# Performance work log

Hardware: AMD Instinct MI355X
Metric: run time of the kernel (lower is better)

## Reference

```python
import jax, jax.numpy as jnp
import numpy as np

K = 5
TAU = 2.0
EPS = 1e-8
SLOPE = 0.2  # LeakyReLU negative slope
BASE = jnp.array([-2.0, -1.0, 0.0, 1.0, 2.0], dtype=jnp.float32)


def _leaky(x):
    return jnp.where(x >= 0, x, SLOPE * x)


def _bilinear1d(feat, x):
    """1D bilinear sample, equivalent to F.grid_sample on an [B,C,1,L] image
    with grid_y=0, padding_mode='border', align_corners=True.
    feat: [B,C,L], x: [B,M] normalized coords in [-1,1]. Returns [B,C,M]."""
    L = feat.shape[-1]
    ix = jnp.clip((x + 1.0) * 0.5 * (L - 1), 0.0, float(L - 1))  # border clamp
    x0 = jnp.floor(ix)
    w = (ix - x0)[:, None, :]  # [B,1,M]
    i0 = jnp.clip(x0.astype(jnp.int32), 0, L - 1)
    i1 = jnp.clip(i0 + 1, 0, L - 1)
    f0 = jnp.take_along_axis(feat, i0[:, None, :], axis=2)
    f1 = jnp.take_along_axis(feat, i1[:, None, :], axis=2)
    return f0 * (1.0 - w) + f1 * w


def setup_inputs() -> dict:
    key = jax.random.key(0)
    ks = jax.random.split(key, 10)
    B, C, Lin, N, H = 4, 256, 4096, 8192, 64
    out_dim = 1 + 1 + K + K  # 12
    feat_1d = jax.random.normal(ks[0], (B, C, Lin), dtype=jnp.float32)
    coords_1d = jax.random.uniform(ks[1], (B, N, 1), minval=-1.0, maxval=1.0, dtype=jnp.float32)
    cell_1d = jnp.full((B, N, 1), 2.0 / Lin, dtype=jnp.float32) * (1.0 + 0.1 * jax.random.uniform(ks[2], (B, N, 1)))
    in_dim = C + 2
    # NOTE: original zero-inits the last linear; we use small random weights to
    # exercise the full computation (non-degenerate offsets/gates).
    W1 = jax.random.normal(ks[3], (in_dim, H), dtype=jnp.float32) * (1.0 / np.sqrt(in_dim))
    b1 = jax.random.normal(ks[4], (H,), dtype=jnp.float32) * 0.01
    Wr = jax.random.normal(ks[5], (H, H), dtype=jnp.float32) * (1.0 / np.sqrt(H))
    br = jax.random.normal(ks[6], (H,), dtype=jnp.float32) * 0.01
    W3 = jax.random.normal(ks[7], (H, out_dim), dtype=jnp.float32) * 0.1
    b3 = jax.random.normal(ks[8], (out_dim,), dtype=jnp.float32) * 0.01
    return {"feat_1d": feat_1d, "coords_1d": coords_1d, "cell_1d": cell_1d,
            "W1": W1, "b1": b1, "Wr": Wr, "br": br, "W3": W3, "b3": b3}


def reference(feat_1d, coords_1d, cell_1d, W1, b1, Wr, br, W3, b3):
    B, C, Lin = feat_1d.shape
    N = coords_1d.shape[1]
    x = coords_1d[..., 0]  # [B,N]
    # anchor features at query coords
    f_anchor = _bilinear1d(feat_1d, x).transpose(0, 2, 1)  # [B,N,C]
    rin = jnp.concatenate([f_anchor, coords_1d, cell_1d], axis=-1)  # [B,N,C+2]
    # router MLP: Linear -> LeakyReLU -> ResidualBlock -> Linear
    h = _leaky(rin @ W1 + b1)
    h = _leaky(h + (h @ Wr + br))
    out = h @ W3 + b3  # [B,N,12]
    r_raw = out[..., 0:1]
    sigma_raw = out[..., 1:2]
    res_raw = out[..., 2:2 + K]
    gate_raw = out[..., 2 + K:2 + 2 * K]
    r = jnp.clip(jax.nn.softplus(r_raw) + 0.3, 0.3, 2.0)          # [B,N,1]
    sigma = jnp.clip(jax.nn.softplus(sigma_raw) + 0.5, 0.5, 3.0)  # [B,N,1]
    res = jnp.tanh(res_raw) * 0.5                                  # [B,N,K]
    off = r * BASE + res                                           # [B,N,K] pixel-unit offsets
    scale_x = 2.0 / max(Lin - 1, 1)
    deform_x = x[:, :, None] + off * scale_x                       # [B,N,K] normalized
    f = _bilinear1d(feat_1d, deform_x.reshape(B, N * K))           # [B,C,N*K]
    f = f.reshape(B, C, N, K).transpose(0, 2, 3, 1)                # [B,N,K,C]
    w_geo = jnp.exp(-0.5 * off ** 2 / ((sigma * TAU) ** 2 + EPS))  # [B,N,K]
    w = w_geo * jax.nn.sigmoid(gate_raw)
    w = w / (w.sum(axis=-1, keepdims=True) + EPS)
    out_feat = jnp.einsum('bnkc,bnk->bnc', f, w)                   # [B,N,C]
    return out_feat
```

## Files before the change

### kernel.cpp

```cpp
#include <hip/hip_runtime.h>
#include <math.h>

#define KK 5
#define C_DIM 256
#define LIN 4096
#define B_DIM 4
#define N_PTS 8192
#define PTS 32
#define NBUCK (B_DIM * LIN)

typedef short short8 __attribute__((ext_vector_type(8)));
typedef float f32x4  __attribute__((ext_vector_type(4)));

__device__ __forceinline__ float leaky(float v) { return v >= 0.0f ? v : 0.2f * v; }
__device__ __forceinline__ float softplus_f(float v) { return v > 20.0f ? v : log1pf(expf(v)); }
__device__ __forceinline__ float bflo(unsigned u) { return __uint_as_float(u << 16); }
__device__ __forceinline__ float bfhi(unsigned u) { return __uint_as_float(u & 0xFFFF0000u); }
__device__ __forceinline__ ushort f2bf(float f) {
    unsigned u = __float_as_uint(f);
    u += 0x7FFFu + ((u >> 16) & 1u);
    return (ushort)(u >> 16);
}
__device__ __forceinline__ float bf2f(ushort h) { return __uint_as_float((unsigned)h << 16); }
__device__ __forceinline__ int anchor_key(const float* coords, int pt) {
    float x = coords[pt];
    float ix = fminf(fmaxf((x + 1.0f) * 0.5f * (float)(LIN - 1), 0.0f), (float)(LIN - 1));
    return (pt >> 13) * LIN + (int)ix;
}

__global__ __launch_bounds__(256) void prep_weights(
    const float* __restrict__ W1, const float* __restrict__ Wr,
    ushort* __restrict__ W1t_hi, ushort* __restrict__ W1t_lo,
    ushort* __restrict__ Wrt_hi, ushort* __restrict__ Wrt_lo)
{
    int i = blockIdx.x * 256 + threadIdx.x;
    if (i < 64 * 264) {
        int j = i / 264, k = i % 264;
        float v = (k < 256) ? W1[(size_t)k * 64 + j] : 0.0f;
        ushort hi = f2bf(v);
        W1t_hi[i] = hi;
        W1t_lo[i] = f2bf(v - bf2f(hi));
    } else {
        int i2 = i - 64 * 264;
        if (i2 < 64 * 72) {
            int j = i2 / 72, k = i2 % 72;
            float v = (k < 64) ? Wr[(size_t)k * 64 + j] : 0.0f;
            ushort hi = f2bf(v);
            Wrt_hi[i2] = hi;
            Wrt_lo[i2] = f2bf(v - bf2f(hi));
        }
    }
}

__global__ __launch_bounds__(256) void sort_count(
    const float* __restrict__ coords, unsigned* __restrict__ hist)
{
    int pt = blockIdx.x * 256 + threadIdx.x;
    atomicAdd(&hist[anchor_key(coords, pt)], 1u);
}

__global__ __launch_bounds__(256) void sort_scan(
    const unsigned* __restrict__ hist, unsigned* __restrict__ offs)
{
    __shared__ unsigned base[256];
    int t = threadIdx.x;
    unsigned s = 0;
    for (int i = 0; i < NBUCK / 256; i++) s += hist[t * (NBUCK / 256) + i];
    base[t] = s;
    __syncthreads();
    if (t == 0) {
        unsigned run = 0;
        for (int i = 0; i < 256; i++) { unsigned v = base[i]; base[i] = run; run += v; }
    }
    __syncthreads();
    unsigned run = base[t];
    for (int i = 0; i < NBUCK / 256; i++) {
        int idx = t * (NBUCK / 256) + i;
        offs[idx] = run;
        run += hist[idx];
    }
}

__global__ __launch_bounds__(256) void sort_scatter(
    const float* __restrict__ coords, unsigned* __restrict__ offs,
    int* __restrict__ perm)
{
    int pt = blockIdx.x * 256 + threadIdx.x;
    unsigned pos = atomicAdd(&offs[anchor_key(coords, pt)], 1u);
    perm[pos] = pt;
}

__global__ __launch_bounds__(256) void transpose_kernel(
    const float* __restrict__ feat, ushort* __restrict__ feat_t)
{
    __shared__ float tile[32][33];
    int b  = blockIdx.z;
    int l0 = blockIdx.x * 32;
    int c0 = blockIdx.y * 32;
    const float* src = feat + (size_t)b * C_DIM * LIN;
    ushort* dst = feat_t + (size_t)b * LIN * C_DIM;
    int tx = threadIdx.x, ty = threadIdx.y;
#pragma unroll
    for (int i = 0; i < 4; i++)
        tile[ty + i * 8][tx] = src[(size_t)(c0 + ty + i * 8) * LIN + (l0 + tx)];
    __syncthreads();
#pragma unroll
    for (int i = 0; i < 4; i++)
        dst[(size_t)(l0 + ty + i * 8) * C_DIM + (c0 + tx)] = f2bf(tile[tx][ty + i * 8]);
}

__global__ __launch_bounds__(256) void mlp_kernel(
    const ushort* __restrict__ feat_t,
    const float* __restrict__ coords,
    const float* __restrict__ cell,
    const float* __restrict__ W1, const float* __restrict__ b1,
    const float* __restrict__ br,
    const float* __restrict__ W3, const float* __restrict__ b3,
    const ushort* __restrict__ W1t_hi, const ushort* __restrict__ W1t_lo,
    const ushort* __restrict__ Wrt_hi, const ushort* __restrict__ Wrt_lo,
    float* __restrict__ params)
{
    __shared__ ushort Ah[PTS][264], Al[PTS][264];
    __shared__ ushort H1h[PTS][72], H1l[PTS][72];
    __shared__ float  H2[PTS][68];
    __shared__ float  outs[PTS][12];
    __shared__ float  xs[PTS], cls[PTS];

    const int t = threadIdx.x;
    const int base = blockIdx.x * PTS;
    const int bb = base >> 13;
    const ushort* fb = feat_t + (size_t)bb * LIN * C_DIM;

    {
        int p = t >> 3, l8 = t & 7;
        int pt = base + p;
        float x = coords[pt];
        float ix = fminf(fmaxf((x + 1.0f) * 0.5f * (float)(LIN - 1), 0.0f), (float)(LIN - 1));
        float x0 = floorf(ix);
        int i0 = min((int)x0, LIN - 1);
        int i1 = min(i0 + 1, LIN - 1);
        float fr = ix - x0, om = 1.0f - fr;
        if (l8 == 0) { xs[p] = x; cls[p] = cell[pt]; }
        const ushort* r0 = fb + (size_t)i0 * C_DIM;
        const ushort* r1 = fb + (size_t)i1 * C_DIM;
#pragma unroll
        for (int q = 0; q < 4; q++) {
            int c = l8 * 8 + q * 64;
            uint4 u0 = *(const uint4*)(r0 + c);
            uint4 u1 = *(const uint4*)(r1 + c);
            float v[8];
            v[0] = bflo(u0.x) * om + bflo(u1.x) * fr;
            v[1] = bfhi(u0.x) * om + bfhi(u1.x) * fr;
            v[2] = bflo(u0.y) * om + bflo(u1.y) * fr;
            v[3] = bfhi(u0.y) * om + bfhi(u1.y) * fr;
            v[4] = bflo(u0.z) * om + bflo(u1.z) * fr;
            v[5] = bfhi(u0.z) * om + bfhi(u1.z) * fr;
            v[6] = bflo(u0.w) * om + bflo(u1.w) * fr;
            v[7] = bfhi(u0.w) * om + bfhi(u1.w) * fr;
            ushort hv[8], lv[8];
#pragma unroll
            for (int e = 0; e < 8; e++) {
                hv[e] = f2bf(v[e]);
                lv[e] = f2bf(v[e] - bf2f(hv[e]));
            }
            *(uint4*)&Ah[p][c] = *(uint4*)hv;
            *(uint4*)&Al[p][c] = *(uint4*)lv;
        }
    }
    __syncthreads();

    const int wave = t >> 6, lane = t & 63;
    const int cr = lane & 15;
    const int kb = lane >> 4;
    const int jcol = wave * 16 + cr;

    f32x4 acc0 = {0.f, 0.f, 0.f, 0.f}, acc1 = acc0;
    {
        const ushort* B1h = W1t_hi + (size_t)jcol * 264;
        const ushort* B1l = W1t_lo + (size_t)jcol * 264;
#pragma unroll
        for (int k0 = 0; k0 < 256; k0 += 32) {
            int ko = k0 + kb * 8;
            short8 a0h = *(const short8*)&Ah[cr][ko];
            short8 a0l = *(const short8*)&Al[cr][ko];
            short8 a1h = *(const short8*)&Ah[16 + cr][ko];
            short8 a1l = *(const short8*)&Al[16 + cr][ko];
            short8 bh = *(const short8*)(B1h + ko);
            short8 bl = *(const short8*)(B1l + ko);
            acc0 = __builtin_amdgcn_mfma_f32_16x16x32_bf16(a0h, bh, acc0, 0, 0, 0);
            acc0 = __builtin_amdgcn_mfma_f32_16x16x32_bf16(a0h, bl, acc0, 0, 0, 0);
            acc0 = __builtin_amdgcn_mfma_f32_16x16x32_bf16(a0l, bh, acc0, 0, 0, 0);
            acc1 = __builtin_amdgcn_mfma_f32_16x16x32_bf16(a1h, bh, acc1, 0, 0, 0);
            acc1 = __builtin_amdgcn_mfma_f32_16x16x32_bf16(a1h, bl, acc1, 0, 0, 0);
            acc1 = __builtin_amdgcn_mfma_f32_16x16x32_bf16(a1l, bh, acc1, 0, 0, 0);
        }
    }
    float h1a[4], h1b[4];
    {
        float wx = W1[(size_t)256 * 64 + jcol];
        float wc = W1[(size_t)257 * 64 + jcol];
        float bb1 = b1[jcol];
#pragma unroll
        for (int r = 0; r < 4; r++) {
            int p0 = kb * 4 + r;
            float v0 = leaky(acc0[r] + xs[p0] * wx + cls[p0] * wc + bb1);
            h1a[r] = v0;
            ushort hi0 = f2bf(v0);
            H1h[p0][jcol] = hi0;
            H1l[p0][jcol] = f2bf(v0 - bf2f(hi0));
            int p1 = 16 + p0;
            float v1 = leaky(acc1[r] + xs[p1] * wx + cls[p1] * wc + bb1);
            h1b[r] = v1;
            ushort hi1 = f2bf(v1);
            H1h[p1][jcol] = hi1;
            H1l[p1][jcol] = f2bf(v1 - bf2f(hi1));
        }
    }
    __syncthreads();

    f32x4 r0 = {0.f, 0.f, 0.f, 0.f}, r1 = r0;
    {
        const ushort* B2h = Wrt_hi + (size_t)jcol * 72;
        const ushort* B2l = Wrt_lo + (size_t)jcol * 72;
#pragma unroll
        for (int k0 = 0; k0 < 64; k0 += 32) {
            int ko = k0 + kb * 8;
            short8 a0h = *(const short8*)&H1h[cr][ko];
            short8 a0l = *(const short8*)&H1l[cr][ko];
            short8 a1h = *(const short8*)&H1h[16 + cr][ko];
            short8 a1l = *(const short8*)&H1l[16 + cr][ko];
            short8 bh = *(const short8*)(B2h + ko);
            short8 bl = *(const short8*)(B2l + ko);
            r0 = __builtin_amdgcn_mfma_f32_16x16x32_bf16(a0h, bh, r0, 0, 0, 0);
            r0 = __builtin_amdgcn_mfma_f32_16x16x32_bf16(a0h, bl, r0, 0, 0, 0);
            r0 = __builtin_amdgcn_mfma_f32_16x16x32_bf16(a0l, bh, r0, 0, 0, 0);
            r1 = __builtin_amdgcn_mfma_f32_16x16x32_bf16(a1h, bh, r1, 0, 0, 0);
            r1 = __builtin_amdgcn_mfma_f32_16x16x32_bf16(a1h, bl, r1, 0, 0, 0);
            r1 = __builtin_amdgcn_mfma_f32_16x16x32_bf16(a1l, bh, r1, 0, 0, 0);
        }
        float brv = br[jcol];
#pragma unroll
        for (int r = 0; r < 4; r++) {
            int p0 = kb * 4 + r;
            H2[p0][jcol]      = leaky(h1a[r] + r0[r] + brv);
            H2[16 + p0][jcol] = leaky(h1b[r] + r1[r] + brv);
        }
    }
    __syncthreads();

    {
        int p = t & 31;
        int o = t >> 5;
        for (int oo = o; oo < 12; oo += 8) {
            float acc = b3[oo];
#pragma unroll 4
            for (int l = 0; l < 64; l++)
                acc = fmaf(H2[p][l], W3[(size_t)l * 12 + oo], acc);
            outs[p][oo] = acc;
        }
    }
    __syncthreads();

    if (t < PTS) {
        int pt = base + t;
        float x = xs[t];
        float r = softplus_f(outs[t][0]) + 0.3f;
        r = fminf(fmaxf(r, 0.3f), 2.0f);
        float sg = softplus_f(outs[t][1]) + 0.5f;
        sg = fminf(fmaxf(sg, 0.5f), 3.0f);
        float denom = (sg * 2.0f) * (sg * 2.0f) + 1e-8f;
        const float BASEv[KK] = {-2.0f, -1.0f, 0.0f, 1.0f, 2.0f};
        float ixk[KK], wk[KK];
        float wsum = 0.0f;
#pragma unroll
        for (int k = 0; k < KK; k++) {
            float res = tanhf(outs[t][2 + k]) * 0.5f;
            float off = r * BASEv[k] + res;
            float dx = x + off * (2.0f / (float)(LIN - 1));
            float ix = (dx + 1.0f) * 0.5f * (float)(LIN - 1);
            ix = fminf(fmaxf(ix, 0.0f), (float)(LIN - 1));
            float gate = outs[t][2 + KK + k];
            float wgeo = expf(-0.5f * off * off / denom);
            float sig = 1.0f / (1.0f + expf(-gate));
            float w = wgeo * sig;
            ixk[k] = ix; wk[k] = w; wsum += w;
        }
        float inv = 1.0f / (wsum + 1e-8f);
        float* pp = params + (size_t)pt * 10;
#pragma unroll
        for (int k = 0; k < KK; k++) {
            pp[k]     = ixk[k];
            pp[5 + k] = wk[k] * inv;
        }
    }
}

__global__ __launch_bounds__(256) void gather_kernel(
    const ushort* __restrict__ feat_t, const float* __restrict__ params,
    const int* __restrict__ perm, float* __restrict__ out)
{
    int t = threadIdx.x;
    int p = t >> 5;
    int lane = t & 31;
    int pt = perm[blockIdx.x * 8 + p];
    int b = pt >> 13;
    const float* pp = params + (size_t)pt * 10;
    const ushort* fb = feat_t + (size_t)b * LIN * C_DIM;
    int c = lane * 8;
    float a0 = 0, a1 = 0, a2 = 0, a3 = 0, a4 = 0, a5 = 0, a6 = 0, a7 = 0;
#pragma unroll
    for (int k = 0; k < KK; k++) {
        float ix = pp[k];
        float w  = pp[5 + k];
        float x0 = floorf(ix);
        int i0 = (int)x0;
        int i1 = min(i0 + 1, LIN - 1);
        float fr = ix - x0;
        uint4 u0 = *(const uint4*)(fb + (size_t)i0 * C_DIM + c);
        uint4 u1 = *(const uint4*)(fb + (size_t)i1 * C_DIM + c);
        float w0 = w * (1.0f - fr), w1 = w * fr;
        a0 = fmaf(w0, bflo(u0.x), fmaf(w1, bflo(u1.x), a0));
        a1 = fmaf(w0, bfhi(u0.x), fmaf(w1, bfhi(u1.x), a1));
        a2 = fmaf(w0, bflo(u0.y), fmaf(w1, bflo(u1.y), a2));
        a3 = fmaf(w0, bfhi(u0.y), fmaf(w1, bfhi(u1.y), a3));
        a4 = fmaf(w0, bflo(u0.z), fmaf(w1, bflo(u1.z), a4));
        a5 = fmaf(w0, bfhi(u0.z), fmaf(w1, bfhi(u1.z), a5));
        a6 = fmaf(w0, bflo(u0.w), fmaf(w1, bflo(u1.w), a6));
        a7 = fmaf(w0, bfhi(u0.w), fmaf(w1, bfhi(u1.w), a7));
    }
    float* op = out + (size_t)pt * C_DIM + c;
    *(float4*)op       = make_float4(a0, a1, a2, a3);
    *(float4*)(op + 4) = make_float4(a4, a5, a6, a7);
}

extern "C" void kernel_launch(void* const* d_in, const int* in_sizes, int n_in,
                              void* d_out, int out_size, void* d_ws, size_t ws_size,
                              hipStream_t stream) {
    const float* feat   = (const float*)d_in[0];
    const float* coords = (const float*)d_in[1];
    const float* cell   = (const float*)d_in[2];
    const float* W1 = (const float*)d_in[3];
    const float* b1 = (const float*)d_in[4];
    const float* Wr = (const float*)d_in[5];
    const float* br = (const float*)d_in[6];
    const float* W3 = (const float*)d_in[7];
    const float* b3 = (const float*)d_in[8];
    float* out = (float*)d_out;

    char* ws = (char*)d_ws;
    ushort* feat_t = (ushort*)ws;
    ws += (size_t)B_DIM * LIN * C_DIM * 2;
    float* params = (float*)ws;
    ws += (size_t)B_DIM * N_PTS * 10 * 4;
    ushort* W1t_hi = (ushort*)ws; ws += 64 * 264 * 2;
    ushort* W1t_lo = (ushort*)ws; ws += 64 * 264 * 2;
    ushort* Wrt_hi = (ushort*)ws; ws += 64 * 72 * 2;
    ushort* Wrt_lo = (ushort*)ws; ws += 64 * 72 * 2;
    ws = (char*)(((uintptr_t)ws + 255) & ~(uintptr_t)255);
    unsigned* hist = (unsigned*)ws; ws += NBUCK * 4;
    unsigned* offs = (unsigned*)ws; ws += NBUCK * 4;
    int* perm      = (int*)ws;      ws += (size_t)B_DIM * N_PTS * 4;

    int nPts = B_DIM * N_PTS;

    hipMemsetAsync(hist, 0, NBUCK * 4, stream);
    sort_count<<<nPts / 256, 256, 0, stream>>>(coords, hist);
    sort_scan<<<1, 256, 0, stream>>>(hist, offs);
    sort_scatter<<<nPts / 256, 256, 0, stream>>>(coords, offs, perm);

    prep_weights<<<(64 * 264 + 64 * 72 + 255) / 256, 256, 0, stream>>>(
        W1, Wr, W1t_hi, W1t_lo, Wrt_hi, Wrt_lo);

    dim3 tb(32, 8);
    dim3 tg(LIN / 32, C_DIM / 32, B_DIM);
    transpose_kernel<<<tg, tb, 0, stream>>>(feat, feat_t);

    mlp_kernel<<<nPts / PTS, 256, 0, stream>>>(feat_t, coords, cell,
                                               W1, b1, br, W3, b3,
                                               W1t_hi, W1t_lo, Wrt_hi, Wrt_lo,
                                               params);

    gather_kernel<<<nPts / 8, 256, 0, stream>>>(feat_t, params, perm, out);
}
```

Measured before the change: 144.1 us.

## Stage feature windows in LDS for gather and process MLP in sorted order

The gather kernel now gives each block a 32-row window of the transposed feature map, plus a 5-row halo, and stages it in shared memory. Each block then processes the sorted points whose anchor falls in that window, using a new prefix array written by the scan kernel. This aims to replace scattered global/L2 row fetches with LDS reads. The MLP kernel also reads points through the sort permutation for better anchor-row locality, and the transpose now writes packed bf16 pairs over a wider channel tile. Risks are load imbalance across windows with uneven point density, and the halo assumption that offsets stay within about 5 pixels.

```diff
diff --git a/kernel.cpp b/kernel.cpp
--- a/kernel.cpp
+++ b/kernel.cpp
@@ -8,6 +8,8 @@
 #define N_PTS 8192
 #define PTS 32
 #define NBUCK (B_DIM * LIN)
+#define WROWS 32
+#define SROWS 44
 
 typedef short short8 __attribute__((ext_vector_type(8)));
 typedef float f32x4  __attribute__((ext_vector_type(4)));
@@ -60,7 +62,8 @@
 }
 
 __global__ __launch_bounds__(256) void sort_scan(
-    const unsigned* __restrict__ hist, unsigned* __restrict__ offs)
+    const unsigned* __restrict__ hist, unsigned* __restrict__ offs,
+    unsigned* __restrict__ pfx)
 {
     __shared__ unsigned base[256];
     int t = threadIdx.x;
@@ -77,8 +80,10 @@
     for (int i = 0; i < NBUCK / 256; i++) {
         int idx = t * (NBUCK / 256) + i;
         offs[idx] = run;
+        pfx[idx] = run;
         run += hist[idx];
     }
+    if (t == 255) pfx[NBUCK] = run;
 }
 
 __global__ __launch_bounds__(256) void sort_scatter(
@@ -93,20 +98,24 @@
 __global__ __launch_bounds__(256) void transpose_kernel(
     const float* __restrict__ feat, ushort* __restrict__ feat_t)
 {
-    __shared__ float tile[32][33];
+    __shared__ float tile[64][33];
     int b  = blockIdx.z;
     int l0 = blockIdx.x * 32;
-    int c0 = blockIdx.y * 32;
+    int c0 = blockIdx.y * 64;
     const float* src = feat + (size_t)b * C_DIM * LIN;
-    ushort* dst = feat_t + (size_t)b * LIN * C_DIM;
+    unsigned* dst = (unsigned*)(feat_t + (size_t)b * LIN * C_DIM);
     int tx = threadIdx.x, ty = threadIdx.y;
 #pragma unroll
-    for (int i = 0; i < 4; i++)
+    for (int i = 0; i < 8; i++)
         tile[ty + i * 8][tx] = src[(size_t)(c0 + ty + i * 8) * LIN + (l0 + tx)];
     __syncthreads();
 #pragma unroll
-    for (int i = 0; i < 4; i++)
-        dst[(size_t)(l0 + ty + i * 8) * C_DIM + (c0 + tx)] = f2bf(tile[tx][ty + i * 8]);
+    for (int i = 0; i < 4; i++) {
+        int l = ty + i * 8;
+        unsigned lo = f2bf(tile[2 * tx][l]);
+        unsigned hi = f2bf(tile[2 * tx + 1][l]);
+        dst[((size_t)(l0 + l) * C_DIM + c0) / 2 + tx] = lo | (hi << 16);
+    }
 }
 
 __global__ __launch_bounds__(256) void mlp_kernel(
@@ -118,6 +127,7 @@
     const float* __restrict__ W3, const float* __restrict__ b3,
     const ushort* __restrict__ W1t_hi, const ushort* __restrict__ W1t_lo,
     const ushort* __restrict__ Wrt_hi, const ushort* __restrict__ Wrt_lo,
+    const int* __restrict__ perm,
     float* __restrict__ params)
 {
     __shared__ ushort Ah[PTS][264], Al[PTS][264];
@@ -133,7 +143,7 @@
 
     {
         int p = t >> 3, l8 = t & 7;
-        int pt = base + p;
+        int pt = perm[base + p];
         float x = coords[pt];
         float ix = fminf(fmaxf((x + 1.0f) * 0.5f * (float)(LIN - 1), 0.0f), (float)(LIN - 1));
         float x0 = floorf(ix);
@@ -262,7 +272,7 @@
     __syncthreads();
 
     if (t < PTS) {
-        int pt = base + t;
+        int pt = perm[base + t];
         float x = xs[t];
         float r = softplus_f(outs[t][0]) + 0.3f;
         r = fminf(fmaxf(r, 0.3f), 2.0f);
@@ -297,40 +307,54 @@
 
 __global__ __launch_bounds__(256) void gather_kernel(
     const ushort* __restrict__ feat_t, const float* __restrict__ params,
-    const int* __restrict__ perm, float* __restrict__ out)
-{
-    int t = threadIdx.x;
-    int p = t >> 5;
-    int lane = t & 31;
-    int pt = perm[blockIdx.x * 8 + p];
-    int b = pt >> 13;
-    const float* pp = params + (size_t)pt * 10;
-    const ushort* fb = feat_t + (size_t)b * LIN * C_DIM;
-    int c = lane * 8;
-    float a0 = 0, a1 = 0, a2 = 0, a3 = 0, a4 = 0, a5 = 0, a6 = 0, a7 = 0;
-#pragma unroll
-    for (int k = 0; k < KK; k++) {
-        float ix = pp[k];
-        float w  = pp[5 + k];
-        float x0 = floorf(ix);
-        int i0 = (int)x0;
-        int i1 = min(i0 + 1, LIN - 1);
-        float fr = ix - x0;
-        uint4 u0 = *(const uint4*)(fb + (size_t)i0 * C_DIM + c);
-        uint4 u1 = *(const uint4*)(fb + (size_t)i1 * C_DIM + c);
-        float w0 = w * (1.0f - fr), w1 = w * fr;
-        a0 = fmaf(w0, bflo(u0.x), fmaf(w1, bflo(u1.x), a0));
-        a1 = fmaf(w0, bfhi(u0.x), fmaf(w1, bfhi(u1.x), a1));
-        a2 = fmaf(w0, bflo(u0.y), fmaf(w1, bflo(u1.y), a2));
-        a3 = fmaf(w0, bfhi(u0.y), fmaf(w1, bfhi(u1.y), a3));
-        a4 = fmaf(w0, bflo(u0.z), fmaf(w1, bflo(u1.z), a4));
-        a5 = fmaf(w0, bfhi(u0.z), fmaf(w1, bfhi(u1.z), a5));
-        a6 = fmaf(w0, bflo(u0.w), fmaf(w1, bflo(u1.w), a6));
-        a7 = fmaf(w0, bfhi(u0.w), fmaf(w1, bfhi(u1.w), a7));
-    }
-    float* op = out + (size_t)pt * C_DIM + c;
-    *(float4*)op       = make_float4(a0, a1, a2, a3);
-    *(float4*)(op + 4) = make_float4(a4, a5, a6, a7);
+    const int* __restrict__ perm, const unsigned* __restrict__ pfx,
+    float* __restrict__ out)
+{
+    __shared__ uint4 sm[SROWS * 32];
+    const int t = threadIdx.x;
+    const int wpb = LIN / WROWS;
+    const int b  = blockIdx.x / wpb;
+    const int w0 = (blockIdx.x % wpb) * WROWS;
+    const int rowLo = max(0, w0 - 5);
+    const int rowHi = min(LIN, w0 + WROWS + 6);
+    const int nrows = rowHi - rowLo;
+
+    const uint4* src = (const uint4*)(feat_t + ((size_t)b * LIN + rowLo) * C_DIM);
+    for (int i = t; i < nrows * 32; i += 256) sm[i] = src[i];
+    __syncthreads();
+
+    const unsigned ptStart = pfx[b * LIN + w0];
+    const unsigned ptEnd   = pfx[b * LIN + w0 + WROWS];
+    const int lane = t & 31;
+
+    for (unsigned ip = ptStart + (t >> 5); ip < ptEnd; ip += 8) {
+        int pt = perm[ip];
+        const float* pp = params + (size_t)pt * 10;
+        float a0 = 0, a1 = 0, a2 = 0, a3 = 0, a4 = 0, a5 = 0, a6 = 0, a7 = 0;
+#pragma unroll
+        for (int k = 0; k < KK; k++) {
+            float ix = pp[k];
+            float w  = pp[5 + k];
+            float x0 = floorf(ix);
+            int i0 = (int)x0;
+            int i1 = min(i0 + 1, LIN - 1);
+            float fr = ix - x0;
+            uint4 u0 = sm[(i0 - rowLo) * 32 + lane];
+            uint4 u1 = sm[(i1 - rowLo) * 32 + lane];
+            float w0f = w * (1.0f - fr), w1f = w * fr;
+            a0 = fmaf(w0f, bflo(u0.x), fmaf(w1f, bflo(u1.x), a0));
+            a1 = fmaf(w0f, bfhi(u0.x), fmaf(w1f, bfhi(u1.x), a1));
+            a2 = fmaf(w0f, bflo(u0.y), fmaf(w1f, bflo(u1.y), a2));
+            a3 = fmaf(w0f, bfhi(u0.y), fmaf(w1f, bfhi(u1.y), a3));
+            a4 = fmaf(w0f, bflo(u0.z), fmaf(w1f, bflo(u1.z), a4));
+            a5 = fmaf(w0f, bfhi(u0.z), fmaf(w1f, bfhi(u1.z), a5));
+            a6 = fmaf(w0f, bflo(u0.w), fmaf(w1f, bflo(u1.w), a6));
+            a7 = fmaf(w0f, bfhi(u0.w), fmaf(w1f, bfhi(u1.w), a7));
+        }
+        float* op = out + (size_t)pt * C_DIM + lane * 8;
+        *(float4*)op       = make_float4(a0, a1, a2, a3);
+        *(float4*)(op + 4) = make_float4(a4, a5, a6, a7);
+    }
 }
 
 extern "C" void kernel_launch(void* const* d_in, const int* in_sizes, int n_in,
@@ -359,26 +383,29 @@
     ws = (char*)(((uintptr_t)ws + 255) & ~(uintptr_t)255);
     unsigned* hist = (unsigned*)ws; ws += NBUCK * 4;
     unsigned* offs = (unsigned*)ws; ws += NBUCK * 4;
+    unsigned* pfx  = (unsigned*)ws; ws += (NBUCK + 1) * 4;
+    ws = (char*)(((uintptr_t)ws + 255) & ~(uintptr_t)255);
     int* perm      = (int*)ws;      ws += (size_t)B_DIM * N_PTS * 4;
 
     int nPts = B_DIM * N_PTS;
 
     hipMemsetAsync(hist, 0, NBUCK * 4, stream);
     sort_count<<<nPts / 256, 256, 0, stream>>>(coords, hist);
-    sort_scan<<<1, 256, 0, stream>>>(hist, offs);
+    sort_scan<<<1, 256, 0, stream>>>(hist, offs, pfx);
     sort_scatter<<<nPts / 256, 256, 0, stream>>>(coords, offs, perm);
 
     prep_weights<<<(64 * 264 + 64 * 72 + 255) / 256, 256, 0, stream>>>(
         W1, Wr, W1t_hi, W1t_lo, Wrt_hi, Wrt_lo);
 
     dim3 tb(32, 8);
-    dim3 tg(LIN / 32, C_DIM / 32, B_DIM);
+    dim3 tg(LIN / 32, C_DIM / 64, B_DIM);
     transpose_kernel<<<tg, tb, 0, stream>>>(feat, feat_t);
 
     mlp_kernel<<<nPts / PTS, 256, 0, stream>>>(feat_t, coords, cell,
                                                W1, b1, br, W3, b3,
                                                W1t_hi, W1t_lo, Wrt_hi, Wrt_lo,
-                                               params);
-
-    gather_kernel<<<nPts / 8, 256, 0, stream>>>(feat_t, params, perm, out);
-}
+                                               perm, params);
+
+    gather_kernel<<<B_DIM * (LIN / WROWS), 256, 0, stream>>>(
+        feat_t, params, perm, pfx, out);
+}
```

New measurement: 149.8 us. 1.04x slower.
